# Kernel tuning notes

Measured on AMD Instinct MI355X. Metric: run time of the kernel, lower is better.

The kernel has to match this reference:

```python
import jax, jax.numpy as jnp
import numpy as np

N = 8192
F_IN = 256
F_OUT = 256
EDGE_P = 0.002  # avg degree ~16 before self-loops


def setup_inputs() -> dict:
    key = jax.random.key(0)
    k_a, k_x, k_w, k_b = jax.random.split(key, 4)
    # symmetric 0/1 dense adjacency, no self loops (added in reference as I + A)
    u = jax.random.uniform(k_a, (N, N))
    A = (u < EDGE_P).astype(jnp.float32)
    A = jnp.maximum(A, A.T)
    A = A * (1.0 - jnp.eye(N, dtype=jnp.float32))
    inputs = jax.random.normal(k_x, (N, F_IN), dtype=jnp.float32)
    # matches torch init: rand/100 - 0.005 in [-0.005, 0.005)
    weight = jax.random.uniform(k_w, (F_IN, F_OUT), dtype=jnp.float32) / 100.0 - 0.005
    bias = jax.random.uniform(k_b, (F_OUT,), dtype=jnp.float32) / 100.0 - 0.005
    return {"A": A, "inputs": inputs, "weight": weight, "bias": bias}


def reference(A, inputs, weight, bias):
    # A_ = I + A
    A_ = A + jnp.eye(A.shape[0], dtype=A.dtype)
    # D^{-1/2}: the original builds diag matrices and does dense GEMMs;
    # row/col scaling is the same math, expressed efficiently.
    d = jnp.sum(A_, axis=1) ** (-0.5)  # [N]
    norm_A = d[:, None] * A_ * d[None, :]  # D^{-1/2} (I+A) D^{-1/2}
    out = norm_A @ inputs @ weight + bias  # [N, F_OUT]
    return out  # activation is None
```

## Files before the change

kernel.cpp:

```cpp
#include <hip/hip_runtime.h>
#include <hip/hip_bf16.h>
#include <cstdint>


#define NN 8192
#define FF 256
#define ELLK 128
#define BM 64
#define BN 64
#define BK 16
#define NGEMM ((NN / BM) * (FF / BN))

__device__ __forceinline__ float bf2f(unsigned short u) {
    union { unsigned int i; float f; } c; c.i = ((unsigned int)u) << 16; return c.f;
}
__device__ __forceinline__ unsigned short f2bf(float f) {
    union { float f; unsigned int i; } c; c.f = f;
    unsigned int r = c.i + 0x7FFF + ((c.i >> 16) & 1);
    return (unsigned short)(r >> 16);
}

__global__ __launch_bounds__(256) void fused_stage1(const float* __restrict__ A,
                                                    const float* __restrict__ X,
                                                    const float* __restrict__ W,
                                                    unsigned short* __restrict__ Yb,
                                                    float* __restrict__ dvals,
                                                    int* __restrict__ nnz,
                                                    unsigned short* __restrict__ ell) {
    if (blockIdx.x < NGEMM) {
        __shared__ float As[BK][BM + 4];
        __shared__ float Bs[BK][BN];
        const int bid = blockIdx.x;
        const int m0 = (bid / (FF / BN)) * BM;
        const int n0 = (bid % (FF / BN)) * BN;
        const int tid = threadIdx.x;
        const int tr = tid / 16;
        const int tc = tid % 16;
        float acc[4][4] = {};
        for (int k0 = 0; k0 < FF; k0 += BK) {
            {
                int r  = tid / 4;
                int kq = (tid % 4) * 4;
                float4 v = *reinterpret_cast<const float4*>(X + (size_t)(m0 + r) * FF + k0 + kq);
                As[kq + 0][r] = v.x; As[kq + 1][r] = v.y; As[kq + 2][r] = v.z; As[kq + 3][r] = v.w;
            }
            {
                int kk = tid / 16;
                int nq = (tid % 16) * 4;
                float4 v = *reinterpret_cast<const float4*>(W + (size_t)(k0 + kk) * FF + n0 + nq);
                *reinterpret_cast<float4*>(&Bs[kk][nq]) = v;
            }
            __syncthreads();
            #pragma unroll
            for (int kk = 0; kk < BK; ++kk) {
                float a[4], b[4];
                #pragma unroll
                for (int i = 0; i < 4; ++i) a[i] = As[kk][tr * 4 + i];
                #pragma unroll
                for (int j = 0; j < 4; ++j) b[j] = Bs[kk][tc * 4 + j];
                #pragma unroll
                for (int i = 0; i < 4; ++i)
                    #pragma unroll
                    for (int j = 0; j < 4; ++j)
                        acc[i][j] = fmaf(a[i], b[j], acc[i][j]);
            }
            __syncthreads();
        }
        #pragma unroll
        for (int i = 0; i < 4; ++i) {
            ushort4 v = { f2bf(acc[i][0]), f2bf(acc[i][1]), f2bf(acc[i][2]), f2bf(acc[i][3]) };
            *reinterpret_cast<ushort4*>(Yb + (size_t)(m0 + tr * 4 + i) * FF + n0 + tc * 4) = v;
        }
    } else {
        __shared__ int cnt;
        __shared__ unsigned short loc[ELLK];
        const int row = blockIdx.x - NGEMM;
        if (threadIdx.x == 0) cnt = 0;
        __syncthreads();
        const uint4* Arow = reinterpret_cast<const uint4*>(A + (size_t)row * NN);
        #pragma unroll
        for (int k = 0; k < 8; ++k) {
            int idx4 = k * 256 + threadIdx.x;
            uint4 v = Arow[idx4];
            int base = idx4 * 4;
            if (v.x) { int p = atomicAdd(&cnt, 1); if (p < ELLK) loc[p] = (unsigned short)(base + 0); }
            if (v.y) { int p = atomicAdd(&cnt, 1); if (p < ELLK) loc[p] = (unsigned short)(base + 1); }
            if (v.z) { int p = atomicAdd(&cnt, 1); if (p < ELLK) loc[p] = (unsigned short)(base + 2); }
            if (v.w) { int p = atomicAdd(&cnt, 1); if (p < ELLK) loc[p] = (unsigned short)(base + 3); }
        }
        __syncthreads();
        int c = cnt < ELLK ? cnt : ELLK;
        for (int t = threadIdx.x; t < c; t += 256)
            ell[(size_t)row * ELLK + t] = loc[t];
        if (threadIdx.x == 0) {
            nnz[row] = c;
            dvals[row] = 1.0f / sqrtf((float)(c + 1));
        }
    }
}

__global__ __launch_bounds__(256) void spmm_kernel(const unsigned short* __restrict__ Yb,
                                                   const float* __restrict__ dvals,
                                                   const int* __restrict__ nnz,
                                                   const unsigned short* __restrict__ ell,
                                                   const float* __restrict__ bias,
                                                   float* __restrict__ out) {
    const int wave = threadIdx.x >> 6;
    const int lane = threadIdx.x & 63;
    const int row = blockIdx.x * 4 + wave;
    __shared__ unsigned short sidx[4][ELLK];
    __shared__ float sdj[4][ELLK];
    const int c = nnz[row];
    for (int t = lane; t < c; t += 64) {
        int j = ell[(size_t)row * ELLK + t];
        sidx[wave][t] = (unsigned short)j;
        sdj[wave][t]  = dvals[j];
    }
    __syncthreads();
    const float di = dvals[row];
    ushort4 ys = *reinterpret_cast<const ushort4*>(Yb + (size_t)row * FF + lane * 4);
    float a0 = di * bf2f(ys.x), a1 = di * bf2f(ys.y);
    float a2 = di * bf2f(ys.z), a3 = di * bf2f(ys.w);
    for (int t = 0; t < c; ++t) {
        int j = sidx[wave][t];
        float dj = sdj[wave][t];
        ushort4 v = *reinterpret_cast<const ushort4*>(Yb + (size_t)j * FF + lane * 4);
        a0 = fmaf(dj, bf2f(v.x), a0);
        a1 = fmaf(dj, bf2f(v.y), a1);
        a2 = fmaf(dj, bf2f(v.z), a2);
        a3 = fmaf(dj, bf2f(v.w), a3);
    }
    float4 b4 = *reinterpret_cast<const float4*>(bias + lane * 4);
    float4 o;
    o.x = fmaf(di, a0, b4.x);
    o.y = fmaf(di, a1, b4.y);
    o.z = fmaf(di, a2, b4.z);
    o.w = fmaf(di, a3, b4.w);
    *reinterpret_cast<float4*>(out + (size_t)row * FF + lane * 4) = o;
}

extern "C" void kernel_launch(void* const* d_in, const int* in_sizes, int n_in,
                              void* d_out, int out_size, void* d_ws, size_t ws_size,
                              hipStream_t stream) {
    const float* A    = (const float*)d_in[0];
    const float* X    = (const float*)d_in[1];
    const float* W    = (const float*)d_in[2];
    const float* bias = (const float*)d_in[3];
    float* out = (float*)d_out;

    char* ws = (char*)d_ws;
    unsigned short* Yb    = (unsigned short*)(ws);
    float*          dvals = (float*)(ws + (size_t)NN * FF * 2);
    int*            nnz   = (int*)(ws + (size_t)NN * FF * 2 + NN * 4);
    unsigned short* ell   = (unsigned short*)(ws + (size_t)NN * FF * 2 + NN * 8);

    fused_stage1<<<NGEMM + NN, 256, 0, stream>>>(A, X, W, Yb, dvals, nnz, ell);
    spmm_kernel<<<NN / 4, 256, 0, stream>>>(Yb, dvals, nnz, ell, bias, out);
}
```

Before: 65.27 us.

## Exploit adjacency symmetry to scan only upper triangle with global atomics

```diff
diff --git a/kernel.cpp b/kernel.cpp
--- a/kernel.cpp
+++ b/kernel.cpp
@@ -10,6 +10,7 @@
 #define BN 64
 #define BK 16
 #define NGEMM ((NN / BM) * (FF / BN))
+#define NSCAN (NN / 2)
 
 __device__ __forceinline__ float bf2f(unsigned short u) {
     union { unsigned int i; float f; } c; c.i = ((unsigned int)u) << 16; return c.f;
@@ -20,12 +21,33 @@
     return (unsigned short)(r >> 16);
 }
 
+__device__ __forceinline__ void scan_row_upper(const float* __restrict__ A, int r,
+                                               int* __restrict__ cnt,
+                                               unsigned short* __restrict__ ell) {
+    const uint4* Arow = reinterpret_cast<const uint4*>(A + (size_t)r * NN);
+    const int c0 = (r + 1) >> 2;
+    for (int c = c0 + threadIdx.x; c < NN / 4; c += 256) {
+        uint4 v = Arow[c];
+        int base = c * 4;
+        #pragma unroll
+        for (int e = 0; e < 4; ++e) {
+            unsigned int ve = (e == 0) ? v.x : (e == 1) ? v.y : (e == 2) ? v.z : v.w;
+            int j = base + e;
+            if (ve && j > r) {
+                int p = atomicAdd(&cnt[r], 1);
+                if (p < ELLK) ell[(size_t)r * ELLK + p] = (unsigned short)j;
+                int q = atomicAdd(&cnt[j], 1);
+                if (q < ELLK) ell[(size_t)j * ELLK + q] = (unsigned short)r;
+            }
+        }
+    }
+}
+
 __global__ __launch_bounds__(256) void fused_stage1(const float* __restrict__ A,
                                                     const float* __restrict__ X,
                                                     const float* __restrict__ W,
                                                     unsigned short* __restrict__ Yb,
-                                                    float* __restrict__ dvals,
-                                                    int* __restrict__ nnz,
+                                                    int* __restrict__ cnt,
                                                     unsigned short* __restrict__ ell) {
     if (blockIdx.x < NGEMM) {
         __shared__ float As[BK][BM + 4];
@@ -39,10 +61,10 @@
         float acc[4][4] = {};
         for (int k0 = 0; k0 < FF; k0 += BK) {
             {
-                int r  = tid / 4;
+                int rr = tid / 4;
                 int kq = (tid % 4) * 4;
-                float4 v = *reinterpret_cast<const float4*>(X + (size_t)(m0 + r) * FF + k0 + kq);
-                As[kq + 0][r] = v.x; As[kq + 1][r] = v.y; As[kq + 2][r] = v.z; As[kq + 3][r] = v.w;
+                float4 v = *reinterpret_cast<const float4*>(X + (size_t)(m0 + rr) * FF + k0 + kq);
+                As[kq + 0][rr] = v.x; As[kq + 1][rr] = v.y; As[kq + 2][rr] = v.z; As[kq + 3][rr] = v.w;
             }
             {
                 int kk = tid / 16;
@@ -72,36 +94,14 @@
             *reinterpret_cast<ushort4*>(Yb + (size_t)(m0 + tr * 4 + i) * FF + n0 + tc * 4) = v;
         }
     } else {
-        __shared__ int cnt;
-        __shared__ unsigned short loc[ELLK];
-        const int row = blockIdx.x - NGEMM;
-        if (threadIdx.x == 0) cnt = 0;
-        __syncthreads();
-        const uint4* Arow = reinterpret_cast<const uint4*>(A + (size_t)row * NN);
-        #pragma unroll
-        for (int k = 0; k < 8; ++k) {
-            int idx4 = k * 256 + threadIdx.x;
-            uint4 v = Arow[idx4];
-            int base = idx4 * 4;
-            if (v.x) { int p = atomicAdd(&cnt, 1); if (p < ELLK) loc[p] = (unsigned short)(base + 0); }
-            if (v.y) { int p = atomicAdd(&cnt, 1); if (p < ELLK) loc[p] = (unsigned short)(base + 1); }
-            if (v.z) { int p = atomicAdd(&cnt, 1); if (p < ELLK) loc[p] = (unsigned short)(base + 2); }
-            if (v.w) { int p = atomicAdd(&cnt, 1); if (p < ELLK) loc[p] = (unsigned short)(base + 3); }
-        }
-        __syncthreads();
-        int c = cnt < ELLK ? cnt : ELLK;
-        for (int t = threadIdx.x; t < c; t += 256)
-            ell[(size_t)row * ELLK + t] = loc[t];
-        if (threadIdx.x == 0) {
-            nnz[row] = c;
-            dvals[row] = 1.0f / sqrtf((float)(c + 1));
-        }
+        const int s = blockIdx.x - NGEMM;
+        scan_row_upper(A, s, cnt, ell);
+        scan_row_upper(A, NN - 1 - s, cnt, ell);
     }
 }
 
 __global__ __launch_bounds__(256) void spmm_kernel(const unsigned short* __restrict__ Yb,
-                                                   const float* __restrict__ dvals,
-                                                   const int* __restrict__ nnz,
+                                                   const int* __restrict__ cnt,
                                                    const unsigned short* __restrict__ ell,
                                                    const float* __restrict__ bias,
                                                    float* __restrict__ out) {
@@ -110,14 +110,15 @@
     const int row = blockIdx.x * 4 + wave;
     __shared__ unsigned short sidx[4][ELLK];
     __shared__ float sdj[4][ELLK];
-    const int c = nnz[row];
+    int c = cnt[row];
+    c = c < ELLK ? c : ELLK;
     for (int t = lane; t < c; t += 64) {
         int j = ell[(size_t)row * ELLK + t];
         sidx[wave][t] = (unsigned short)j;
-        sdj[wave][t]  = dvals[j];
+        sdj[wave][t]  = rsqrtf((float)(cnt[j] + 1));
     }
     __syncthreads();
-    const float di = dvals[row];
+    const float di = rsqrtf((float)(cnt[row] + 1));
     ushort4 ys = *reinterpret_cast<const ushort4*>(Yb + (size_t)row * FF + lane * 4);
     float a0 = di * bf2f(ys.x), a1 = di * bf2f(ys.y);
     float a2 = di * bf2f(ys.z), a3 = di * bf2f(ys.w);
@@ -149,11 +150,12 @@
     float* out = (float*)d_out;
 
     char* ws = (char*)d_ws;
-    unsigned short* Yb    = (unsigned short*)(ws);
-    float*          dvals = (float*)(ws + (size_t)NN * FF * 2);
-    int*            nnz   = (int*)(ws + (size_t)NN * FF * 2 + NN * 4);
-    unsigned short* ell   = (unsigned short*)(ws + (size_t)NN * FF * 2 + NN * 8);
+    unsigned short* Yb  = (unsigned short*)(ws);
+    int*            cnt = (int*)(ws + (size_t)NN * FF * 2);
+    unsigned short* ell = (unsigned short*)(ws + (size_t)NN * FF * 2 + NN * 4);
 
-    fused_stage1<<<NGEMM + NN, 256, 0, stream>>>(A, X, W, Yb, dvals, nnz, ell);
-    spmm_kernel<<<NN / 4, 256, 0, stream>>>(Yb, dvals, nnz, ell, bias, out);
+    hipMemsetAsync(cnt, 0, NN * sizeof(int), stream);
+
+    fused_stage1<<<NGEMM + NSCAN, 256, 0, stream>>>(A, X, W, Yb, cnt, ell);
+    spmm_kernel<<<NN / 4, 256, 0, stream>>>(Yb, cnt, ell, bias, out);
 }
```

Result: slower. 68.84 us (+5.5%).
